# Kernel optimization log

Hardware: AMD Instinct MI355X
Metric: run time of the kernel (lower is better)

The kernel has to match this reference:

```python
import jax, jax.numpy as jnp
import numpy as np

EMBED_DIM = 2048
NUM_HEADS = 16
BLOCK_SIZE = 128


def setup_inputs() -> dict:
    key = jax.random.key(0)
    k1, k2, k3 = jax.random.split(key, 3)
    B, S, E = 2, 4096, EMBED_DIM
    x = jax.random.normal(k1, (B, S, E), dtype=jnp.float32)
    # small init so attention logits are in a sane range
    w_qkv = jax.random.normal(k2, (3 * E, E), dtype=jnp.float32) * 0.02
    w_out = jax.random.normal(k3, (E, E), dtype=jnp.float32) * 0.02
    b_out = jnp.zeros((E,), dtype=jnp.float32)
    return {"x": x, "w_qkv": w_qkv, "w_out": w_out, "b_out": b_out}


def _flash_attention_v2(q, k, v, block_size, scale):
    # q,k,v: [B,H,S,D]; S divisible by block_size.
    # Faithful to the torch module, including its extra l_ij factor in the
    # output rescaling (out += beta*l_ij/l_new * (p @ v)).
    B, H, S, D = q.shape
    nb = S // block_size
    qb = q.reshape(B, H, nb, block_size, D)          # all query blocks at once
    kb = k.reshape(B, H, nb, block_size, D).transpose(2, 0, 1, 3, 4)  # [nb,B,H,bs,D]
    vb = v.reshape(B, H, nb, block_size, D).transpose(2, 0, 1, 3, 4)

    out0 = jnp.zeros_like(qb)
    l0 = jnp.zeros((B, H, nb, block_size, 1), dtype=q.dtype)
    m0 = jnp.full((B, H, nb, block_size, 1), -jnp.inf, dtype=q.dtype)

    def step(carry, kv):
        out, l, m = carry
        k_j, v_j = kv  # [B,H,bs,D]
        s = jnp.einsum('bhnqd,bhkd->bhnqk', qb, k_j) * scale  # [B,H,nb,bs,bs]
        m_ij = jnp.max(s, axis=-1, keepdims=True)
        p = jnp.exp(s - m_ij)
        l_ij = jnp.sum(p, axis=-1, keepdims=True)
        m_new = jnp.maximum(m, m_ij)
        alpha = jnp.exp(m - m_new)
        beta = jnp.exp(m_ij - m_new)
        l_new = alpha * l + beta * l_ij
        pv = jnp.einsum('bhnqk,bhkd->bhnqd', p, v_j)
        out_new = (alpha * l / l_new) * out + (beta * l_ij / l_new) * pv
        return (out_new, l_new, m_new), None

    (out, _, _), _ = jax.lax.scan(step, (out0, l0, m0), (kb, vb))
    return out.reshape(B, H, S, D)


def reference(x, w_qkv, w_out, b_out):
    B, S, E = x.shape
    H = NUM_HEADS
    D = E // H
    scale = 1.0 / np.sqrt(D).astype(np.float32)
    qkv = (x @ w_qkv.T).reshape(B, S, 3, H, D)
    q, k, v = jnp.moveaxis(qkv, 2, 0)            # each [B,S,H,D]
    q = q.transpose(0, 2, 1, 3)                   # [B,H,S,D]
    k = k.transpose(0, 2, 1, 3)
    v = v.transpose(0, 2, 1, 3)
    out = _flash_attention_v2(q, k, v, BLOCK_SIZE, scale)  # [B,H,S,D]
    out = out.transpose(0, 2, 1, 3).reshape(B, S, E)
    return out @ w_out.T + b_out
```

## Files before the change

### kernel.cpp

```cpp
#include <hip/hip_runtime.h>
#include <hip/hip_bf16.h>
#include <stdint.h>

#define DEV __device__ __forceinline__

typedef __attribute__((ext_vector_type(8))) short short8;
typedef __attribute__((ext_vector_type(4))) float f32x4;

#define B_ 2
#define S_ 4096
#define E_ 2048
#define H_ 16
#define D_ 128

DEV unsigned short f2bf(float x) {
  union { float f; uint32_t u; } a; a.f = x;
  uint32_t r = a.u + 0x7fffu + ((a.u >> 16) & 1u);
  return (unsigned short)(r >> 16);
}

DEV unsigned int cvt_pk_bf16(float a, float b) {
  unsigned int r;
  asm("v_cvt_pk_bf16_f32 %0, %1, %2" : "=v"(r) : "v"(a), "v"(b));
  return r;
}

DEV float exp2f_(float x) { return __builtin_amdgcn_exp2f(x); }

DEV void glds16(const void* g, void* l) {
  __builtin_amdgcn_global_load_lds(
      (const __attribute__((address_space(1))) uint32_t*)g,
      (__attribute__((address_space(3))) uint32_t*)l, 16, 0, 0);
}

__global__ __launch_bounds__(256) void cvtk(const float* __restrict__ in,
                                            unsigned short* __restrict__ out, int n4) {
  int i = blockIdx.x * blockDim.x + threadIdx.x;
  int stride = gridDim.x * blockDim.x;
  for (; i < n4; i += stride) {
    float4 v = ((const float4*)in)[i];
    ushort4 o;
    o.x = f2bf(v.x); o.y = f2bf(v.y); o.z = f2bf(v.z); o.w = f2bf(v.w);
    ((ushort4*)out)[i] = o;
  }
}

template<int OUT_F32>
__global__ __launch_bounds__(256) void gemm_nt(
    const unsigned short* __restrict__ A,
    const unsigned short* __restrict__ Bm,
    void* __restrict__ Cp,
    const float* __restrict__ bias,
    int M, int N, int K, int nbn)
{
  __shared__ __align__(16) unsigned char lA[128 * 64];
  __shared__ __align__(16) unsigned char lB[128 * 64];
  int bid = blockIdx.x;
  int bm = bid / nbn, bn = bid % nbn;
  int t = threadIdx.x;
  int lane = t & 63, wv = t >> 6;
  int hi = lane >> 4, lo = lane & 15;
  int wm = wv >> 1, wn = wv & 1;
  int m0 = bm * 128, n0 = bn * 128;

  f32x4 acc[4][4] = {};

  for (int k0 = 0; k0 < K; k0 += 32) {
#pragma unroll
    for (int i = 0; i < 2; ++i) {
      int slot = i * 256 + t;
      int row = slot >> 2, c = slot & 3;
      int lbase = (i * 256 + wv * 64) * 16;
      glds16(A + (size_t)(m0 + row) * K + k0 + c * 8, lA + lbase);
      glds16(Bm + (size_t)(n0 + row) * K + k0 + c * 8, lB + lbase);
    }
    __syncthreads();
    short8 af[4], bfr[4];
#pragma unroll
    for (int mi = 0; mi < 4; ++mi)
      af[mi] = *(const short8*)(lA + (wm * 64 + mi * 16 + lo) * 64 + hi * 16);
#pragma unroll
    for (int nj = 0; nj < 4; ++nj)
      bfr[nj] = *(const short8*)(lB + (wn * 64 + nj * 16 + lo) * 64 + hi * 16);
#pragma unroll
    for (int mi = 0; mi < 4; ++mi)
#pragma unroll
      for (int nj = 0; nj < 4; ++nj)
        acc[mi][nj] = __builtin_amdgcn_mfma_f32_16x16x32_bf16(af[mi], bfr[nj], acc[mi][nj], 0, 0, 0);
    __syncthreads();
  }

  if constexpr (OUT_F32) {
    float* C = (float*)Cp;
#pragma unroll
    for (int mi = 0; mi < 4; ++mi)
#pragma unroll
      for (int nj = 0; nj < 4; ++nj) {
        int row = m0 + wm * 64 + mi * 16 + hi * 4;
        int col = n0 + wn * 64 + nj * 16 + lo;
        float bv = bias[col];
#pragma unroll
        for (int r = 0; r < 4; ++r)
          C[(size_t)(row + r) * N + col] = acc[mi][nj][r] + bv;
      }
  } else {
    unsigned short* C = (unsigned short*)Cp;
#pragma unroll
    for (int mi = 0; mi < 4; ++mi)
#pragma unroll
      for (int nj = 0; nj < 4; ++nj) {
        int row = m0 + wm * 64 + mi * 16 + hi * 4;
        int col = n0 + wn * 64 + nj * 16 + lo;
#pragma unroll
        for (int r = 0; r < 4; ++r)
          C[(size_t)(row + r) * N + col] = f2bf(acc[mi][nj][r]);
      }
  }
}

__global__ __launch_bounds__(256) void transpose_v(const unsigned short* __restrict__ qkv,
                                                   unsigned short* __restrict__ vt) {
  __shared__ __align__(16) unsigned char tl[32768];
  int bid = blockIdx.x;
  int st = bid & 31, bh = bid >> 5;
  int h = bh & 15, b = bh >> 4;
  int s0 = st * 128;
  int t = threadIdx.x, c = t & 15, rr = t >> 4;
#pragma unroll
  for (int i = 0; i < 8; ++i) {
    int s = rr + i * 16;
    const unsigned short* g = qkv + ((((size_t)b * S_ + s0 + s) * 3 + 2) * H_ + h) * D_ + c * 8;
    *(uint4*)(tl + s * 256 + ((c * 16) ^ (((s >> 3) & 7) << 4))) = *(const uint4*)g;
  }
  __syncthreads();
#pragma unroll
  for (int i = 0; i < 8; ++i) {
    int d = rr + i * 16;
    unsigned int w[4];
#pragma unroll
    for (int jj = 0; jj < 4; ++jj) {
      int s_a = c * 8 + jj * 2;
      unsigned int u0 = *(const unsigned short*)(tl + s_a * 256 + ((d * 2) ^ ((c & 7) << 4)));
      unsigned int u1 = *(const unsigned short*)(tl + (s_a + 1) * 256 + ((d * 2) ^ ((c & 7) << 4)));
      w[jj] = u0 | (u1 << 16);
    }
    uint4 val; val.x = w[0]; val.y = w[1]; val.z = w[2]; val.w = w[3];
    unsigned short* g = vt + (((size_t)b * H_ + h) * D_ + d) * S_ + s0 + c * 8;
    *(uint4*)g = val;
  }
}

__global__ __launch_bounds__(512, 2) void attn_fwd(
    const unsigned short* __restrict__ qkv,
    const unsigned short* __restrict__ vt,
    unsigned short* __restrict__ abuf)
{
  __shared__ __align__(16) unsigned char lds[65536];
  unsigned char* lK = lds;
  unsigned char* lV = lds + 32768;

  int bid = (blockIdx.x & 7) * 64 + (blockIdx.x >> 3);
  int qb = bid & 15, bh = bid >> 4;
  int h = bh & 15, b = bh >> 4;
  int t = threadIdx.x, lane = t & 63, wv = t >> 6;
  int hi = lane >> 4, lo = lane & 15;
  int q0 = qb * 256;
  const float c1 = 0.12751744f;

  short8 qf[2][4];
#pragma unroll
  for (int qj = 0; qj < 2; ++qj) {
    const unsigned short* qbase =
        qkv + ((((size_t)b * S_ + q0 + wv * 32 + qj * 16 + lo) * 3 + 0) * H_ + h) * D_;
#pragma unroll
    for (int ks = 0; ks < 4; ++ks)
      qf[qj][ks] = *(const short8*)(qbase + ks * 32 + hi * 8);
  }

  int sw = ((t & 15) * 16) ^ (((t >> 4) & 7) << 4);
  const unsigned char* gkb =
      (const unsigned char*)(qkv + (((size_t)b * S_ * 3 + 1) * H_ + h) * D_) +
      (size_t)(t >> 4) * 12288 + sw;
  const unsigned char* gvb =
      (const unsigned char*)(vt + ((size_t)b * H_ + h) * D_ * S_) +
      (size_t)(t >> 4) * 8192 + sw;
  unsigned char* lkd = lK + wv * 1024;
  unsigned char* lvd = lV + wv * 1024;

  f32x4 oacc[8][2] = {};
  float m_run[2] = {-__builtin_inff(), -__builtin_inff()};
  float l_run[2] = {0.f, 0.f};
  union PW { unsigned int u[4]; short8 s; };
  PW pp[2][4];

#pragma unroll
  for (int i = 0; i < 4; ++i) {
    glds16(gkb + i * 393216, lkd + i * 8192);
    glds16(gvb + i * 262144, lvd + i * 8192);
  }

  for (int jb = 0; jb < 32; ++jb) {
    asm volatile("s_waitcnt vmcnt(0)" ::: "memory");
    asm volatile("s_barrier" ::: "memory");

    f32x4 sacc[8][2];
    __builtin_amdgcn_s_setprio(1);
#pragma unroll
    for (int kf = 0; kf < 8; ++kf) {
      int kvr = kf * 16 + lo;
      int swz = (kvr & 7) << 4;
      sacc[kf][0] = f32x4{0.f, 0.f, 0.f, 0.f};
      sacc[kf][1] = f32x4{0.f, 0.f, 0.f, 0.f};
#pragma unroll
      for (int ks = 0; ks < 4; ++ks) {
        short8 kfr = *(const short8*)(lK + kvr * 256 + ((ks * 64 + hi * 16) ^ swz));
        sacc[kf][0] = __builtin_amdgcn_mfma_f32_16x16x32_bf16(kfr, qf[0][ks], sacc[kf][0], 0, 0, 0);
        sacc[kf][1] = __builtin_amdgcn_mfma_f32_16x16x32_bf16(kfr, qf[1][ks], sacc[kf][1], 0, 0, 0);
      }
    }
    __builtin_amdgcn_s_setprio(0);

    float m2[2], li[2], coef[2];
#pragma unroll
    for (int qj = 0; qj < 2; ++qj) {
      float mloc = -__builtin_inff();
#pragma unroll
      for (int kf = 0; kf < 8; ++kf)
#pragma unroll
        for (int r = 0; r < 4; ++r) mloc = fmaxf(mloc, sacc[kf][qj][r]);
      mloc = fmaxf(mloc, __shfl_xor(mloc, 16));
      mloc = fmaxf(mloc, __shfl_xor(mloc, 32));
      m2[qj] = mloc * c1;
      float lloc = 0.f;
#pragma unroll
      for (int kf = 0; kf < 8; ++kf)
#pragma unroll
        for (int r = 0; r < 4; ++r) {
          float p = exp2f_(fmaf(sacc[kf][qj][r], c1, -m2[qj]));
          sacc[kf][qj][r] = p;
          lloc += p;
        }
      lloc += __shfl_xor(lloc, 16);
      lloc += __shfl_xor(lloc, 32);
      li[qj] = lloc;
    }

    if (__all(m2[0] <= m_run[0] && m2[1] <= m_run[1])) {
#pragma unroll
      for (int qj = 0; qj < 2; ++qj) {
        coef[qj] = exp2f_(m2[qj] - m_run[qj]) * li[qj];
        l_run[qj] += coef[qj];
      }
    } else {
      float alpha[2];
#pragma unroll
      for (int qj = 0; qj < 2; ++qj) {
        float mn = fmaxf(m_run[qj], m2[qj]);
        alpha[qj] = exp2f_(m_run[qj] - mn);
        coef[qj] = exp2f_(m2[qj] - mn) * li[qj];
        l_run[qj] = alpha[qj] * l_run[qj] + coef[qj];
        m_run[qj] = mn;
      }
#pragma unroll
      for (int df = 0; df < 8; ++df)
#pragma unroll
        for (int qj = 0; qj < 2; ++qj)
#pragma unroll
          for (int r = 0; r < 4; ++r) oacc[df][qj][r] *= alpha[qj];
    }

#pragma unroll
    for (int qj = 0; qj < 2; ++qj) {
      float cf = coef[qj];
#pragma unroll
      for (int ks = 0; ks < 4; ++ks) {
        unsigned int a0 = cvt_pk_bf16(sacc[2 * ks][qj][0] * cf, sacc[2 * ks][qj][1] * cf);
        unsigned int b0 = cvt_pk_bf16(sacc[2 * ks + 1][qj][0] * cf, sacc[2 * ks + 1][qj][1] * cf);
        unsigned int a1 = cvt_pk_bf16(sacc[2 * ks][qj][2] * cf, sacc[2 * ks][qj][3] * cf);
        unsigned int b1 = cvt_pk_bf16(sacc[2 * ks + 1][qj][2] * cf, sacc[2 * ks + 1][qj][3] * cf);
        asm("v_permlane32_swap_b32 %0, %1" : "+v"(a0), "+v"(b0));
        asm("v_permlane16_swap_b32 %0, %1" : "+v"(a0), "+v"(b0));
        asm("v_permlane32_swap_b32 %0, %1" : "+v"(a1), "+v"(b1));
        asm("v_permlane16_swap_b32 %0, %1" : "+v"(a1), "+v"(b1));
        pp[qj][ks].u[0] = a0;
        pp[qj][ks].u[1] = a1;
        pp[qj][ks].u[2] = b0;
        pp[qj][ks].u[3] = b1;
      }
    }

    __builtin_amdgcn_s_setprio(1);
#pragma unroll
    for (int ks = 0; ks < 4; ++ks) {
#pragma unroll
      for (int df = 0; df < 8; ++df) {
        int dr = df * 16 + lo;
        short8 vf = *(const short8*)(lV + dr * 256 + ((ks * 64 + hi * 16) ^ ((dr & 7) << 4)));
        oacc[df][0] = __builtin_amdgcn_mfma_f32_16x16x32_bf16(vf, pp[0][ks].s, oacc[df][0], 0, 0, 0);
        oacc[df][1] = __builtin_amdgcn_mfma_f32_16x16x32_bf16(vf, pp[1][ks].s, oacc[df][1], 0, 0, 0);
      }
    }
    __builtin_amdgcn_s_setprio(0);

    asm volatile("s_barrier" ::: "memory");
    if (jb < 31) {
      size_t kvK = (size_t)(jb + 1) * 1572864;
      size_t kvV = (size_t)(jb + 1) * 256;
#pragma unroll
      for (int i = 0; i < 4; ++i) {
        glds16(gkb + kvK + i * 393216, lkd + i * 8192);
        glds16(gvb + kvV + i * 262144, lvd + i * 8192);
      }
    }
  }

  asm volatile("s_barrier" ::: "memory");
#pragma unroll
  for (int qj = 0; qj < 2; ++qj) {
    int rq = wv * 32 + qj * 16 + lo;
    int swzq = (rq & 7) << 4;
    float inv = 1.0f / l_run[qj];
#pragma unroll
    for (int df = 0; df < 8; ++df) {
      uint2 pk;
      pk.x = cvt_pk_bf16(oacc[df][qj][0] * inv, oacc[df][qj][1] * inv);
      pk.y = cvt_pk_bf16(oacc[df][qj][2] * inv, oacc[df][qj][3] * inv);
      *(uint2*)(lds + rq * 256 + ((df * 32 + hi * 8) ^ swzq)) = pk;
    }
  }
  __syncthreads();
#pragma unroll
  for (int i = 0; i < 8; ++i) {
    int row = i * 32 + (t >> 4);
    int c = t & 15;
    uint4 val = *(const uint4*)(lds + row * 256 + ((c * 16) ^ ((row & 7) << 4)));
    unsigned short* dst = abuf + (((size_t)b * S_ + q0 + row) * H_ + h) * D_ + c * 8;
    *(uint4*)dst = val;
  }
}

extern "C" void kernel_launch(void* const* d_in, const int* in_sizes, int n_in,
                              void* d_out, int out_size, void* d_ws, size_t ws_size,
                              hipStream_t stream) {
  const float* x = (const float*)d_in[0];
  const float* w_qkv = (const float*)d_in[1];
  const float* w_out = (const float*)d_in[2];
  const float* b_out = (const float*)d_in[3];
  float* out = (float*)d_out;
  char* ws = (char*)d_ws;

  unsigned short* xb    = (unsigned short*)(ws);
  unsigned short* wqkvb = (unsigned short*)(ws + 33554432);
  unsigned short* woutb = (unsigned short*)(ws + 58720256);
  unsigned short* qkvb  = (unsigned short*)(ws + 67108864);
  unsigned short* vtb   = (unsigned short*)(ws + 167772160);
  unsigned short* abuf  = xb;

  cvtk<<<2048, 256, 0, stream>>>(x, xb, (B_ * S_ * E_) / 4);
  cvtk<<<2048, 256, 0, stream>>>(w_qkv, wqkvb, (3 * E_ * E_) / 4);
  cvtk<<<1024, 256, 0, stream>>>(w_out, woutb, (E_ * E_) / 4);

  gemm_nt<0><<<64 * 48, 256, 0, stream>>>(xb, wqkvb, (void*)qkvb, nullptr,
                                          B_ * S_, 3 * E_, E_, 48);
  transpose_v<<<1024, 256, 0, stream>>>(qkvb, vtb);
  attn_fwd<<<512, 512, 0, stream>>>(qkvb, vtb, abuf);
  gemm_nt<1><<<64 * 16, 256, 0, stream>>>(abuf, woutb, (void*)out, b_out,
                                          B_ * S_, E_, E_, 16);
}
```

Baseline: 755.9 us.

## Replace GEMM with 256x256 tile, double-buffered, swizzled LDS pipelined kernel

Replaces the 128x128, single-buffered, K=32-step GEMM with a 256x256 tile kernel using 8 waves and K=64 tiles. It double-buffers A and B in 128KB of LDS with XOR swizzle and interleaves global-to-LDS prefetch with the MFMA phases using explicit barriers and waitcnts. Blocks are also remapped across 8 groups, likely for XCD-aware L2 locality. This raises data reuse per block and hides load latency, at the cost of fewer blocks and heavy LDS use that limits occupancy.

```diff
diff --git a/kernel.cpp b/kernel.cpp
--- a/kernel.cpp
+++ b/kernel.cpp
@@ -12,6 +12,10 @@
 #define E_ 2048
 #define H_ 16
 #define D_ 128
+
+#define BAR() asm volatile("s_barrier" ::: "memory")
+#define LGKM0() asm volatile("s_waitcnt lgkmcnt(0)" ::: "memory")
+#define VMC(N) asm volatile("s_waitcnt vmcnt(" #N ")" ::: "memory")
 
 DEV unsigned short f2bf(float x) {
   union { float f; uint32_t u; } a; a.f = x;
@@ -46,74 +50,126 @@
 }
 
 template<int OUT_F32>
-__global__ __launch_bounds__(256) void gemm_nt(
+__global__ __launch_bounds__(512, 2) void gemm256(
     const unsigned short* __restrict__ A,
     const unsigned short* __restrict__ Bm,
     void* __restrict__ Cp,
     const float* __restrict__ bias,
     int M, int N, int K, int nbn)
 {
-  __shared__ __align__(16) unsigned char lA[128 * 64];
-  __shared__ __align__(16) unsigned char lB[128 * 64];
-  int bid = blockIdx.x;
+  __shared__ __align__(16) unsigned char lds[131072];
+  const int NT = K >> 6;
+  const int K2 = K * 2;
+  int cpx = gridDim.x >> 3;
+  int bid = (blockIdx.x & 7) * cpx + (blockIdx.x >> 3);
   int bm = bid / nbn, bn = bid % nbn;
-  int t = threadIdx.x;
-  int lane = t & 63, wv = t >> 6;
-  int hi = lane >> 4, lo = lane & 15;
-  int wm = wv >> 1, wn = wv & 1;
-  int m0 = bm * 128, n0 = bn * 128;
-
-  f32x4 acc[4][4] = {};
-
-  for (int k0 = 0; k0 < K; k0 += 32) {
-#pragma unroll
-    for (int i = 0; i < 2; ++i) {
-      int slot = i * 256 + t;
-      int row = slot >> 2, c = slot & 3;
-      int lbase = (i * 256 + wv * 64) * 16;
-      glds16(A + (size_t)(m0 + row) * K + k0 + c * 8, lA + lbase);
-      glds16(Bm + (size_t)(n0 + row) * K + k0 + c * 8, lB + lbase);
-    }
-    __syncthreads();
-    short8 af[4], bfr[4];
-#pragma unroll
-    for (int mi = 0; mi < 4; ++mi)
-      af[mi] = *(const short8*)(lA + (wm * 64 + mi * 16 + lo) * 64 + hi * 16);
-#pragma unroll
-    for (int nj = 0; nj < 4; ++nj)
-      bfr[nj] = *(const short8*)(lB + (wn * 64 + nj * 16 + lo) * 64 + hi * 16);
-#pragma unroll
-    for (int mi = 0; mi < 4; ++mi)
-#pragma unroll
-      for (int nj = 0; nj < 4; ++nj)
-        acc[mi][nj] = __builtin_amdgcn_mfma_f32_16x16x32_bf16(af[mi], bfr[nj], acc[mi][nj], 0, 0, 0);
-    __syncthreads();
+  int m0 = bm * 256, n0 = bn * 256;
+  int t = threadIdx.x, lane = t & 63, wv = t >> 6;
+  int lo = lane & 15, hi = lane >> 4;
+  int wm = wv >> 2, wn = wv & 3;
+
+  int colsw = ((t & 7) * 16) ^ (((t >> 3) & 7) << 4);
+  const unsigned char* gA = (const unsigned char*)A + (size_t)(m0 + (t >> 3)) * K2 + colsw;
+  const unsigned char* gB = (const unsigned char*)Bm + (size_t)(n0 + (t >> 3)) * K2 + colsw;
+
+  int swzl = (lo & 7) << 4;
+  int colk0 = (hi * 16) ^ swzl;
+  int colk1 = (64 + hi * 16) ^ swzl;
+  unsigned char* rdA = lds + wm * 16384 + lo * 128;
+  unsigned char* rdB = lds + 32768 + (wn >> 1) * 16384 + ((wn & 1) * 64 + lo) * 128;
+
+  f32x4 acc[8][4] = {};
+
+  auto STG = [&](int isA, int d, int h, int kt) {
+    if (kt >= NT) return;
+    const unsigned char* g = (isA ? gA : gB) + (size_t)h * 128 * K2 + (size_t)kt * 128;
+    unsigned char* l = lds + (isA ? 0 : 32768) + d * 65536 + h * 16384 + wv * 1024;
+    glds16(g, l);
+    glds16(g + (size_t)64 * K2, l + 8192);
+  };
+  auto DSA = [&](int d, int g4, int colk, short8* dst) {
+#pragma unroll
+    for (int i = 0; i < 4; ++i)
+      dst[i] = *(const short8*)(rdA + d * 65536 + (g4 * 4 + i) * 2048 + colk);
+  };
+  auto DSB = [&](int d, int colk, short8* dst) {
+#pragma unroll
+    for (int i = 0; i < 4; ++i)
+      dst[i] = *(const short8*)(rdB + d * 65536 + i * 2048 + colk);
+  };
+  auto MM = [&](int g4, short8* a, short8* b) {
+    __builtin_amdgcn_s_setprio(1);
+#pragma unroll
+    for (int i = 0; i < 4; ++i)
+#pragma unroll
+      for (int j = 0; j < 4; ++j)
+        acc[g4 * 4 + i][j] =
+            __builtin_amdgcn_mfma_f32_16x16x32_bf16(a[i], b[j], acc[g4 * 4 + i][j], 0, 0, 0);
+    __builtin_amdgcn_s_setprio(0);
+  };
+
+  STG(1, 0, 0, 0); STG(1, 0, 1, 0); STG(0, 0, 0, 0); STG(0, 0, 1, 0);
+  STG(0, 1, 0, 1); STG(0, 1, 1, 1);
+  VMC(4);
+  BAR();
+
+  short8 aT[4], aU[4], b0[4], b1[4];
+  const int TL = (NT >> 1) - 1;
+  for (int it = 0; it <= TL; ++it) {
+    int j0 = 2 * it;
+    DSA(0, 0, colk0, aT); DSB(0, colk0, b0);
+    STG(1, 1, 0, j0 + 1);
+    BAR(); MM(0, aT, b0); LGKM0(); BAR();
+    DSA(0, 1, colk0, aU); DSB(0, colk1, b1);
+    STG(1, 1, 1, j0 + 1);
+    BAR(); MM(1, aU, b0); LGKM0(); BAR();
+    DSA(0, 0, colk1, aT);
+    STG(0, 0, 0, j0 + 2);
+    BAR(); MM(0, aT, b1); LGKM0(); BAR();
+    DSA(0, 1, colk1, aU);
+    STG(0, 0, 1, j0 + 2);
+    BAR(); MM(1, aU, b1); LGKM0();
+    if (it == TL) { VMC(0); } else { VMC(4); }
+    BAR();
+    DSA(1, 0, colk0, aT); DSB(1, colk0, b0);
+    STG(1, 0, 0, j0 + 2);
+    BAR(); MM(0, aT, b0); LGKM0(); BAR();
+    DSA(1, 1, colk0, aU); DSB(1, colk1, b1);
+    STG(1, 0, 1, j0 + 2);
+    BAR(); MM(1, aU, b0); LGKM0(); BAR();
+    DSA(1, 0, colk1, aT);
+    STG(0, 1, 0, j0 + 3);
+    BAR(); MM(0, aT, b1); LGKM0(); BAR();
+    DSA(1, 1, colk1, aU);
+    STG(0, 1, 1, j0 + 3);
+    BAR(); MM(1, aU, b1); LGKM0(); VMC(4);
+    BAR();
   }
 
   if constexpr (OUT_F32) {
     float* C = (float*)Cp;
 #pragma unroll
-    for (int mi = 0; mi < 4; ++mi)
-#pragma unroll
-      for (int nj = 0; nj < 4; ++nj) {
-        int row = m0 + wm * 64 + mi * 16 + hi * 4;
-        int col = n0 + wn * 64 + nj * 16 + lo;
+    for (int mf = 0; mf < 8; ++mf)
+#pragma unroll
+      for (int nf = 0; nf < 4; ++nf) {
+        int row = m0 + wm * 128 + mf * 16 + hi * 4;
+        int col = n0 + wn * 64 + nf * 16 + lo;
         float bv = bias[col];
 #pragma unroll
         for (int r = 0; r < 4; ++r)
-          C[(size_t)(row + r) * N + col] = acc[mi][nj][r] + bv;
+          C[(size_t)(row + r) * N + col] = acc[mf][nf][r] + bv;
       }
   } else {
     unsigned short* C = (unsigned short*)Cp;
 #pragma unroll
-    for (int mi = 0; mi < 4; ++mi)
-#pragma unroll
-      for (int nj = 0; nj < 4; ++nj) {
-        int row = m0 + wm * 64 + mi * 16 + hi * 4;
-        int col = n0 + wn * 64 + nj * 16 + lo;
+    for (int mf = 0; mf < 8; ++mf)
+#pragma unroll
+      for (int nf = 0; nf < 4; ++nf) {
+        int row = m0 + wm * 128 + mf * 16 + hi * 4;
+        int col = n0 + wn * 64 + nf * 16 + lo;
 #pragma unroll
         for (int r = 0; r < 4; ++r)
-          C[(size_t)(row + r) * N + col] = f2bf(acc[mi][nj][r]);
+          C[(size_t)(row + r) * N + col] = f2bf(acc[mf][nf][r]);
       }
   }
 }
@@ -200,8 +256,8 @@
   }
 
   for (int jb = 0; jb < 32; ++jb) {
-    asm volatile("s_waitcnt vmcnt(0)" ::: "memory");
-    asm volatile("s_barrier" ::: "memory");
+    VMC(0);
+    BAR();
 
     f32x4 sacc[8][2];
     __builtin_amdgcn_s_setprio(1);
@@ -302,7 +358,7 @@
     }
     __builtin_amdgcn_s_setprio(0);
 
-    asm volatile("s_barrier" ::: "memory");
+    BAR();
     if (jb < 31) {
       size_t kvK = (size_t)(jb + 1) * 1572864;
       size_t kvV = (size_t)(jb + 1) * 256;
@@ -314,7 +370,7 @@
     }
   }
 
-  asm volatile("s_barrier" ::: "memory");
+  BAR();
 #pragma unroll
   for (int qj = 0; qj < 2; ++qj) {
     int rq = wv * 32 + qj * 16 + lo;
@@ -360,10 +416,10 @@
   cvtk<<<2048, 256, 0, stream>>>(w_qkv, wqkvb, (3 * E_ * E_) / 4);
   cvtk<<<1024, 256, 0, stream>>>(w_out, woutb, (E_ * E_) / 4);
 
-  gemm_nt<0><<<64 * 48, 256, 0, stream>>>(xb, wqkvb, (void*)qkvb, nullptr,
-                                          B_ * S_, 3 * E_, E_, 48);
+  gemm256<0><<<768, 512, 0, stream>>>(xb, wqkvb, (void*)qkvb, nullptr,
+                                      B_ * S_, 3 * E_, E_, 24);
   transpose_v<<<1024, 256, 0, stream>>>(qkvb, vtb);
   attn_fwd<<<512, 512, 0, stream>>>(qkvb, vtb, abuf);
-  gemm_nt<1><<<64 * 16, 256, 0, stream>>>(abuf, woutb, (void*)out, b_out,
-                                          B_ * S_, E_, E_, 16);
-}
+  gemm256<1><<<256, 512, 0, stream>>>(abuf, woutb, (void*)out, b_out,
+                                      B_ * S_, E_, E_, 8);
+}
```

Result: faster. 637.6 us (-15.7%).
